# Kernel tuning notes

Hardware: AMD Instinct MI355X
Metric: run time of the kernel (lower is better)

Reference implementation:

```python
import jax, jax.numpy as jnp
import numpy as np

B, C, CI, H, W = 4, 64, 32, 96, 96  # batch, in_channels, inter_channels, spatial
EPS = 1e-5


def conv1x1(x, w, b):
    # x: [B,Cin,H,W], w: [Cout,Cin], b: [Cout]
    return jnp.einsum('bchw,oc->bohw', x, w) + b[None, :, None, None]


def maxpool2(x):
    b, c, h, w = x.shape
    return x.reshape(b, c, h // 2, 2, w // 2, 2).max(axis=(3, 5))


def setup_inputs() -> dict:
    key = jax.random.key(0)
    ks = jax.random.split(key, 12)
    s = 0.05  # keep unscaled attention logits in a sane range
    return {
        'x': jax.random.normal(ks[0], (B, C, H, W), jnp.float32),
        'feature': jax.random.normal(ks[1], (B, CI, H, W), jnp.float32),
        'g_w': jax.random.normal(ks[2], (C, C), jnp.float32) * s,
        'g_b': jax.random.normal(ks[3], (C,), jnp.float32) * s,
        'theta_w': jax.random.normal(ks[4], (C, C), jnp.float32) * s,
        'theta_b': jax.random.normal(ks[5], (C,), jnp.float32) * s,
        'phi_w': jax.random.normal(ks[6], (C, CI), jnp.float32) * s,
        'phi_b': jax.random.normal(ks[7], (C,), jnp.float32) * s,
        'W_w': jax.random.normal(ks[8], (CI, C), jnp.float32) * s,
        'W_b': jax.random.normal(ks[9], (CI,), jnp.float32) * s,
        'bn_gamma': jax.random.normal(ks[10], (CI,), jnp.float32) * s + 1.0,
        'bn_beta': jax.random.normal(ks[11], (CI,), jnp.float32) * s,
    }


def reference(x, feature, g_w, g_b, theta_w, theta_b, phi_w, phi_b, W_w, W_b, bn_gamma, bn_beta):
    b = x.shape[0]
    # g branch: conv1x1 then 2x2 maxpool -> [B, M, C]
    g_x = maxpool2(conv1x1(x, g_w, g_b)).reshape(b, C, -1).transpose(0, 2, 1)
    # theta: conv1x1 -> [B, N, C]
    theta_x = conv1x1(x, theta_w, theta_b).reshape(b, C, -1).transpose(0, 2, 1)
    # phi on `feature` (inter_channels -> in_channels) then maxpool -> [B, C, M]
    phi_f = maxpool2(conv1x1(feature, phi_w, phi_b)).reshape(b, C, -1)
    # unscaled attention: [B, N, M]
    f = jnp.einsum('bnc,bcm->bnm', theta_x, phi_f)
    f_div_C = jax.nn.softmax(f, axis=-1)
    y = jnp.einsum('bnm,bmc->bnc', f_div_C, g_x)  # [B, N, C]
    y = y.transpose(0, 2, 1).reshape(x.shape)
    z = y + x
    # W: conv1x1 (C -> CI) + BatchNorm2d (training mode, batch stats)
    z = conv1x1(z, W_w, W_b)
    mean = z.mean(axis=(0, 2, 3), keepdims=True)
    var = z.var(axis=(0, 2, 3), keepdims=True)
    z = (z - mean) * jax.lax.rsqrt(var + EPS)
    z = z * bn_gamma[None, :, None, None] + bn_beta[None, :, None, None]
    return z
```

## Files before the change

### kernel.cpp

```cpp
#include <hip/hip_runtime.h>
#include <hip/hip_bf16.h>

typedef __attribute__((ext_vector_type(8))) short short8;
typedef __attribute__((ext_vector_type(4))) float f32x4;
typedef __attribute__((ext_vector_type(4))) _Float16 half4;

#define NB 4
#define NN 9216
#define NM 2304

__device__ inline unsigned pk2(float a, float b) {
  __hip_bfloat16 ha = __float2bfloat16(a), hb = __float2bfloat16(b);
  return (unsigned)*(unsigned short*)&ha | ((unsigned)*(unsigned short*)&hb << 16);
}
__device__ inline float ubf(unsigned u) {
  unsigned v = u << 16; return *(float*)&v;
}
__device__ inline short8 pack8(const float* v) {
  short8 s;
#pragma unroll
  for (int j = 0; j < 8; ++j) { __hip_bfloat16 h = __float2bfloat16(v[j]); s[j] = *(short*)&h; }
  return s;
}
__device__ inline short8 ldw8(const float* p) {
  float tmp[8];
  *(float4*)&tmp[0] = *(const float4*)p;
  *(float4*)&tmp[4] = *(const float4*)(p + 4);
  return pack8(tmp);
}

__global__ __launch_bounds__(256, 3) void conv_pool_k(
    const float* __restrict__ x, const float* __restrict__ feat,
    const float* __restrict__ tw, const float* __restrict__ tbi,
    const float* __restrict__ gw, const float* __restrict__ gbi,
    const float* __restrict__ pw, const float* __restrict__ pbi,
    __hip_bfloat16* __restrict__ Theta, _Float16* __restrict__ Gcm,
    __hip_bfloat16* __restrict__ PhiT, float* __restrict__ psum) {
  __shared__ float xs[64][68];
  __shared__ float fs[64][36];
  int t = threadIdx.x, wv = t >> 6, lane = t & 63, l15 = lane & 15, q = lane >> 4;
  int b = blockIdx.y, bx = blockIdx.x;
  if (bx == 0 && b == 0 && t < 64) psum[t] = 0.f;
  int jt = bx % 3, rp = bx / 3;
  int i0 = rp * 2, j0 = jt * 32;
  int ot = wv;

  {
#pragma unroll
    for (int p = 0; p < 4; ++p) {
      int idx = p * 256 + t;
      int c = idx >> 4, s = idx & 15;
      int row = s >> 3, cl = (s & 7) * 4;
      float4 v = *(const float4*)(x + ((size_t)b * 64 + c) * NN + (i0 + row) * 96 + j0 + cl);
      int nl = row * 32 + cl;
      xs[nl][c] = v.x; xs[nl + 1][c] = v.y; xs[nl + 2][c] = v.z; xs[nl + 3][c] = v.w;
    }
#pragma unroll
    for (int p = 0; p < 2; ++p) {
      int idx = p * 256 + t;
      int c = idx >> 4, s = idx & 15;
      int row = s >> 3, cl = (s & 7) * 4;
      float4 v = *(const float4*)(feat + ((size_t)b * 32 + c) * NN + (i0 + row) * 96 + j0 + cl);
      int nl = row * 32 + cl;
      fs[nl][c] = v.x; fs[nl + 1][c] = v.y; fs[nl + 2][c] = v.z; fs[nl + 3][c] = v.w;
    }
  }

  short8 wt[2], wg[2], wp1;
#pragma unroll
  for (int kf = 0; kf < 2; ++kf) {
    wt[kf] = ldw8(tw + (size_t)(ot * 16 + l15) * 64 + kf * 32 + q * 8);
    wg[kf] = ldw8(gw + (size_t)(ot * 16 + l15) * 64 + kf * 32 + q * 8);
  }
  wp1 = ldw8(pw + (size_t)(ot * 16 + l15) * 32 + q * 8);

  __syncthreads();

  short8 bxf[4][2], bff[4];
  {
    float tmp[8];
#pragma unroll
    for (int tl = 0; tl < 4; ++tl) {
#pragma unroll
      for (int kf = 0; kf < 2; ++kf) {
        *(float4*)&tmp[0] = *(float4*)&xs[tl * 16 + l15][kf * 32 + q * 8];
        *(float4*)&tmp[4] = *(float4*)&xs[tl * 16 + l15][kf * 32 + q * 8 + 4];
        bxf[tl][kf] = pack8(tmp);
      }
      *(float4*)&tmp[0] = *(float4*)&fs[tl * 16 + l15][q * 8];
      *(float4*)&tmp[4] = *(float4*)&fs[tl * 16 + l15][q * 8 + 4];
      bff[tl] = pack8(tmp);
    }
  }

#pragma unroll
  for (int tl = 0; tl < 4; ++tl) {
    f32x4 d;
#pragma unroll
    for (int r = 0; r < 4; ++r) d[r] = tbi[ot * 16 + q * 4 + r];
    d = __builtin_amdgcn_mfma_f32_16x16x32_bf16(wt[0], bxf[tl][0], d, 0, 0, 0);
    d = __builtin_amdgcn_mfma_f32_16x16x32_bf16(wt[1], bxf[tl][1], d, 0, 0, 0);
    int n = (i0 + (tl >> 1)) * 96 + j0 + (tl & 1) * 16 + l15;
    size_t base = ((size_t)b * NN + n) * 64 + ot * 16 + q * 4;
    *(unsigned*)(Theta + base) = pk2(d[0], d[1]);
    *(unsigned*)(Theta + base + 2) = pk2(d[2], d[3]);
  }

  int mrow = rp * 48 + jt * 16;
  bool em = (l15 & 1) == 0;
#pragma unroll
  for (int ch = 0; ch < 2; ++ch) {
    f32x4 d0, d1;
#pragma unroll
    for (int r = 0; r < 4; ++r) { float bb = gbi[ot * 16 + q * 4 + r]; d0[r] = bb; d1[r] = bb; }
    d0 = __builtin_amdgcn_mfma_f32_16x16x32_bf16(wg[0], bxf[ch][0], d0, 0, 0, 0);
    d0 = __builtin_amdgcn_mfma_f32_16x16x32_bf16(wg[1], bxf[ch][1], d0, 0, 0, 0);
    d1 = __builtin_amdgcn_mfma_f32_16x16x32_bf16(wg[0], bxf[ch + 2][0], d1, 0, 0, 0);
    d1 = __builtin_amdgcn_mfma_f32_16x16x32_bf16(wg[1], bxf[ch + 2][1], d1, 0, 0, 0);
    float h[4];
#pragma unroll
    for (int r = 0; r < 4; ++r) {
      float v = fmaxf(d0[r], d1[r]);
      h[r] = fmaxf(v, __shfl_xor(v, 1));
    }
    if (em) {
      int m = mrow + ch * 8 + (l15 >> 1);
#pragma unroll
      for (int r = 0; r < 4; ++r)
        Gcm[((size_t)b * 64 + ot * 16 + q * 4 + r) * NM + m] = (_Float16)h[r];
    }
  }
#pragma unroll
  for (int ch = 0; ch < 2; ++ch) {
    f32x4 d0, d1;
#pragma unroll
    for (int r = 0; r < 4; ++r) { float bb = pbi[ot * 16 + q * 4 + r]; d0[r] = bb; d1[r] = bb; }
    d0 = __builtin_amdgcn_mfma_f32_16x16x32_bf16(wp1, bff[ch], d0, 0, 0, 0);
    d1 = __builtin_amdgcn_mfma_f32_16x16x32_bf16(wp1, bff[ch + 2], d1, 0, 0, 0);
    float h[4];
#pragma unroll
    for (int r = 0; r < 4; ++r) {
      float v = fmaxf(d0[r], d1[r]);
      h[r] = fmaxf(v, __shfl_xor(v, 1));
    }
    if (em) {
      int m = mrow + ch * 8 + (l15 >> 1);
      size_t base = ((size_t)b * NM + m) * 64 + ot * 16 + q * 4;
      *(unsigned*)(PhiT + base) = pk2(h[0], h[1]);
      *(unsigned*)(PhiT + base + 2) = pk2(h[2], h[3]);
    }
  }
}

__global__ __launch_bounds__(256, 3) void attn_k(
    const __hip_bfloat16* __restrict__ Theta, const __hip_bfloat16* __restrict__ PhiT,
    const _Float16* __restrict__ Gcm, const float* __restrict__ x,
    const float* __restrict__ Ww, const float* __restrict__ Wb,
    float* __restrict__ z2, float* __restrict__ psum) {
  __shared__ union {
    struct { __hip_bfloat16 phis[64][72]; _Float16 gs[64][72]; } st;
    struct { __hip_bfloat16 zpart[4][64][68]; __hip_bfloat16 zacc[64][72]; } ep;
  } u;
  __shared__ float rs[4][64];

  int t = threadIdx.x, wv = t >> 6, lane = t & 63;
  int l15 = lane & 15, q = lane >> 4;
  int b = blockIdx.y;
  int n0 = blockIdx.x * 64;

  short8 tb[4][2];
#pragma unroll
  for (int nt = 0; nt < 4; ++nt)
#pragma unroll
    for (int kf = 0; kf < 2; ++kf)
      tb[nt][kf] = *(const short8*)(Theta + ((size_t)b * NN + n0 + nt * 16 + l15) * 64 + kf * 32 + q * 8);

  f32x4 acc[4][4];
#pragma unroll
  for (int nt = 0; nt < 4; ++nt)
#pragma unroll
    for (int ct = 0; ct < 4; ++ct) acc[nt][ct] = (f32x4){0.f, 0.f, 0.f, 0.f};
  float rsum[4] = {0.f, 0.f, 0.f, 0.f};

  const __hip_bfloat16* phibase = PhiT + (size_t)b * NM * 64;
  const _Float16* gbase = Gcm + (size_t)b * 64 * NM;

  for (int ck = 0; ck < NM / 64; ++ck) {
    int m0 = ck * 64;
    __syncthreads();
#pragma unroll
    for (int p = 0; p < 2; ++p) {
      int idx = p * 256 + t, r = idx >> 3, seg = idx & 7;
      *(uint4*)&u.st.phis[r][seg * 8] = *(const uint4*)(phibase + (size_t)(m0 + r) * 64 + seg * 8);
    }
#pragma unroll
    for (int p = 0; p < 2; ++p) {
      int idx = p * 256 + t, c = idx >> 3, seg = idx & 7;
      *(uint4*)&u.st.gs[c][seg * 8] = *(const uint4*)(gbase + (size_t)c * NM + m0 + seg * 8);
    }
    __syncthreads();

    short8 pha[2];
#pragma unroll
    for (int kf = 0; kf < 2; ++kf)
      pha[kf] = *(const short8*)&u.st.phis[wv * 16 + l15][kf * 32 + q * 8];
    half4 gv[4];
#pragma unroll
    for (int ct = 0; ct < 4; ++ct)
      gv[ct] = *(const half4*)&u.st.gs[ct * 16 + l15][wv * 16 + q * 4];

    half4 pa[4];
#pragma unroll
    for (int nt = 0; nt < 4; ++nt) {
      f32x4 s = (f32x4){0.f, 0.f, 0.f, 0.f};
      s = __builtin_amdgcn_mfma_f32_16x16x32_bf16(pha[0], tb[nt][0], s, 0, 0, 0);
      s = __builtin_amdgcn_mfma_f32_16x16x32_bf16(pha[1], tb[nt][1], s, 0, 0, 0);
      float e0 = __expf(s[0]), e1 = __expf(s[1]), e2 = __expf(s[2]), e3 = __expf(s[3]);
      rsum[nt] += (e0 + e1) + (e2 + e3);
      pa[nt] = (half4){(_Float16)e0, (_Float16)e1, (_Float16)e2, (_Float16)e3};
    }
#pragma unroll
    for (int nt = 0; nt < 4; ++nt)
#pragma unroll
      for (int ct = 0; ct < 4; ++ct)
        acc[nt][ct] = __builtin_amdgcn_mfma_f32_16x16x16f16(pa[nt], gv[ct], acc[nt][ct], 0, 0, 0);
  }

#pragma unroll
  for (int nt = 0; nt < 4; ++nt) {
    float v = rsum[nt];
    v += __shfl_xor(v, 16);
    v += __shfl_xor(v, 32);
    if (lane < 16) rs[wv][nt * 16 + lane] = v;
  }
  __syncthreads();

#pragma unroll
  for (int nt = 0; nt < 4; ++nt)
#pragma unroll
    for (int ct = 0; ct < 4; ++ct)
#pragma unroll
      for (int r = 0; r < 4; ++r)
        u.ep.zpart[wv][nt * 16 + q * 4 + r][ct * 16 + l15] = __float2bfloat16(acc[nt][ct][r]);
  __syncthreads();

  {
    int row = wv * 16 + l15;
    float tot = rs[0][row] + rs[1][row] + rs[2][row] + rs[3][row];
    float rinv = 1.0f / tot;
    float ys[16];
#pragma unroll
    for (int j4 = 0; j4 < 4; ++j4) {
      uint2 p0 = *(const uint2*)&u.ep.zpart[0][row][q * 16 + j4 * 4];
      ys[j4 * 4 + 0] = ubf(p0.x & 0xffffu); ys[j4 * 4 + 1] = ubf(p0.x >> 16);
      ys[j4 * 4 + 2] = ubf(p0.y & 0xffffu); ys[j4 * 4 + 3] = ubf(p0.y >> 16);
    }
#pragma unroll
    for (int wvv = 1; wvv < 4; ++wvv) {
#pragma unroll
      for (int j4 = 0; j4 < 4; ++j4) {
        uint2 p0 = *(const uint2*)&u.ep.zpart[wvv][row][q * 16 + j4 * 4];
        ys[j4 * 4 + 0] += ubf(p0.x & 0xffffu); ys[j4 * 4 + 1] += ubf(p0.x >> 16);
        ys[j4 * 4 + 2] += ubf(p0.y & 0xffffu); ys[j4 * 4 + 3] += ubf(p0.y >> 16);
      }
    }
    float z1[16];
#pragma unroll
    for (int i = 0; i < 16; ++i)
      z1[i] = ys[i] * rinv + x[((size_t)b * 64 + q * 16 + i) * NN + n0 + row];
#pragma unroll
    for (int i2 = 0; i2 < 8; ++i2)
      *(unsigned*)&u.ep.zacc[row][q * 16 + 2 * i2] = pk2(z1[2 * i2], z1[2 * i2 + 1]);
  }
  __syncthreads();

  int nw = n0 + wv * 16;
  short8 wbf[2][2];
#pragma unroll
  for (int ot = 0; ot < 2; ++ot)
#pragma unroll
    for (int kf = 0; kf < 2; ++kf)
      wbf[ot][kf] = ldw8(Ww + (size_t)(ot * 16 + l15) * 64 + kf * 32 + q * 8);
  short8 za0 = *(const short8*)&u.ep.zacc[wv * 16 + l15][q * 8];
  short8 za1 = *(const short8*)&u.ep.zacc[wv * 16 + l15][32 + q * 8];

  f32x4 dd[2];
#pragma unroll
  for (int ot = 0; ot < 2; ++ot) {
    float bias = Wb[ot * 16 + l15];
    f32x4 d = (f32x4){bias, bias, bias, bias};
    d = __builtin_amdgcn_mfma_f32_16x16x32_bf16(za0, wbf[ot][0], d, 0, 0, 0);
    d = __builtin_amdgcn_mfma_f32_16x16x32_bf16(za1, wbf[ot][1], d, 0, 0, 0);
#pragma unroll
    for (int r = 0; r < 4; ++r)
      z2[((size_t)b * NN + nw + q * 4 + r) * 32 + ot * 16 + l15] = d[r];
    dd[ot] = d;
  }

  __syncthreads();
#pragma unroll
  for (int ot = 0; ot < 2; ++ot) {
    float ps = (dd[ot][0] + dd[ot][1]) + (dd[ot][2] + dd[ot][3]);
    float ps2 = dd[ot][0] * dd[ot][0] + dd[ot][1] * dd[ot][1] +
                dd[ot][2] * dd[ot][2] + dd[ot][3] * dd[ot][3];
    ps += __shfl_xor(ps, 16);  ps += __shfl_xor(ps, 32);
    ps2 += __shfl_xor(ps2, 16); ps2 += __shfl_xor(ps2, 32);
    if (lane < 16) {
      rs[wv][ot * 16 + lane] = ps;
      rs[wv][32 + ot * 16 + lane] = ps2;
    }
  }
  __syncthreads();
  if (t < 64) {
    float tot = rs[0][t] + rs[1][t] + rs[2][t] + rs[3][t];
    atomicAdd(&psum[t], tot);
  }
}

__global__ __launch_bounds__(256) void bn_apply(
    const float* __restrict__ z2, const float* __restrict__ psum,
    const float* __restrict__ gamma, const float* __restrict__ beta,
    float* __restrict__ out) {
  __shared__ float ssl[64];
  __shared__ float zt[32][65];
  int t = threadIdx.x, b = blockIdx.y, n0 = blockIdx.x * 64;
  if (t < 32) {
    const float inv = 1.0f / (float)(NB * NN);
    float mean = psum[t] * inv;
    float var = psum[32 + t] * inv - mean * mean;
    float sc = gamma[t] * rsqrtf(var + 1e-5f);
    ssl[t] = sc;
    ssl[32 + t] = beta[t] - mean * sc;
  }
#pragma unroll
  for (int it = 0; it < 2; ++it) {
    int idx = it * 256 + t, r = idx >> 3, seg = idx & 7;
    float4 vv = *(const float4*)(z2 + ((size_t)b * NN + n0 + r) * 32 + seg * 4);
    zt[seg * 4 + 0][r] = vv.x; zt[seg * 4 + 1][r] = vv.y;
    zt[seg * 4 + 2][r] = vv.z; zt[seg * 4 + 3][r] = vv.w;
  }
  __syncthreads();
  int o = t >> 3, nseg = t & 7;
  float sc = ssl[o], sh = ssl[32 + o];
  float4 a, c;
  a.x = zt[o][nseg * 8 + 0] * sc + sh; a.y = zt[o][nseg * 8 + 1] * sc + sh;
  a.z = zt[o][nseg * 8 + 2] * sc + sh; a.w = zt[o][nseg * 8 + 3] * sc + sh;
  c.x = zt[o][nseg * 8 + 4] * sc + sh; c.y = zt[o][nseg * 8 + 5] * sc + sh;
  c.z = zt[o][nseg * 8 + 6] * sc + sh; c.w = zt[o][nseg * 8 + 7] * sc + sh;
  float* po = out + ((size_t)b * 32 + o) * NN + n0 + nseg * 8;
  *(float4*)po = a;
  *(float4*)(po + 4) = c;
}

extern "C" void kernel_launch(void* const* d_in, const int* in_sizes, int n_in,
                              void* d_out, int out_size, void* d_ws, size_t ws_size,
                              hipStream_t stream) {
  const float* x       = (const float*)d_in[0];
  const float* feature = (const float*)d_in[1];
  const float* g_w     = (const float*)d_in[2];
  const float* g_b     = (const float*)d_in[3];
  const float* theta_w = (const float*)d_in[4];
  const float* theta_b = (const float*)d_in[5];
  const float* phi_w   = (const float*)d_in[6];
  const float* phi_b   = (const float*)d_in[7];
  const float* W_w     = (const float*)d_in[8];
  const float* W_b     = (const float*)d_in[9];
  const float* bn_g    = (const float*)d_in[10];
  const float* bn_b    = (const float*)d_in[11];

  char* ws = (char*)d_ws;
  __hip_bfloat16* Theta = (__hip_bfloat16*)(ws);
  _Float16*       Gcm   = (_Float16*)(ws + 4718592);
  __hip_bfloat16* PhiT  = (__hip_bfloat16*)(ws + 5898240);
  float*          z2    = (float*)(ws + 7077888);
  float*          psum  = (float*)(ws + 11796480);

  conv_pool_k<<<dim3(144, NB), dim3(256), 0, stream>>>(
      x, feature, theta_w, theta_b, g_w, g_b, phi_w, phi_b, Theta, Gcm, PhiT, psum);
  attn_k<<<dim3(144, NB), dim3(256), 0, stream>>>(
      Theta, PhiT, Gcm, x, W_w, W_b, z2, psum);
  bn_apply<<<dim3(144, NB), dim3(256), 0, stream>>>(
      z2, psum, bn_g, bn_b, (float*)d_out);
}
```

Before: 148.8 us.

## Fuse three kernels into one persistent kernel with software grid barriers

```diff
diff --git a/kernel.cpp b/kernel.cpp
--- a/kernel.cpp
+++ b/kernel.cpp
@@ -8,6 +8,7 @@
 #define NB 4
 #define NN 9216
 #define NM 2304
+#define NBLK (144 * NB)
 
 __device__ inline unsigned pk2(float a, float b) {
   __hip_bfloat16 ha = __float2bfloat16(a), hb = __float2bfloat16(b);
@@ -29,23 +30,46 @@
   return pack8(tmp);
 }
 
-__global__ __launch_bounds__(256, 3) void conv_pool_k(
+__device__ inline void gridbar(unsigned* c, unsigned target) {
+  __syncthreads();
+  __threadfence();
+  if (threadIdx.x == 0) {
+    atomicAdd(c, 1u);
+    while (atomicAdd(c, 0u) < target) __builtin_amdgcn_s_sleep(8);
+  }
+  __syncthreads();
+  __threadfence();
+}
+
+__global__ __launch_bounds__(256, 3) void mega_k(
     const float* __restrict__ x, const float* __restrict__ feat,
     const float* __restrict__ tw, const float* __restrict__ tbi,
     const float* __restrict__ gw, const float* __restrict__ gbi,
     const float* __restrict__ pw, const float* __restrict__ pbi,
+    const float* __restrict__ Ww, const float* __restrict__ Wb,
+    const float* __restrict__ gamma, const float* __restrict__ beta,
     __hip_bfloat16* __restrict__ Theta, _Float16* __restrict__ Gcm,
-    __hip_bfloat16* __restrict__ PhiT, float* __restrict__ psum) {
-  __shared__ float xs[64][68];
-  __shared__ float fs[64][36];
-  int t = threadIdx.x, wv = t >> 6, lane = t & 63, l15 = lane & 15, q = lane >> 4;
+    __hip_bfloat16* __restrict__ PhiT,
+    unsigned* __restrict__ ctr, float* __restrict__ psum,
+    float* __restrict__ out) {
+  __shared__ union {
+    struct { float xs[64][68]; float fs[64][36]; } cv;
+    struct { __hip_bfloat16 phis[64][72]; _Float16 gs[64][72]; } st;
+    struct { __hip_bfloat16 zpart[4][64][68]; __hip_bfloat16 zacc[64][72]; } ep;
+    float zt[32][68];
+  } u;
+  __shared__ float rs[4][64];
+  __shared__ float ssl[64];
+
+  int t = threadIdx.x, wv = t >> 6, lane = t & 63;
+  int l15 = lane & 15, q = lane >> 4;
   int b = blockIdx.y, bx = blockIdx.x;
-  if (bx == 0 && b == 0 && t < 64) psum[t] = 0.f;
-  int jt = bx % 3, rp = bx / 3;
-  int i0 = rp * 2, j0 = jt * 32;
-  int ot = wv;
 
   {
+    int jt = bx % 3, rp = bx / 3;
+    int i0 = rp * 2, j0 = jt * 32;
+    int ot = wv;
+
 #pragma unroll
     for (int p = 0; p < 4; ++p) {
       int idx = p * 256 + t;
@@ -53,7 +77,8 @@
       int row = s >> 3, cl = (s & 7) * 4;
       float4 v = *(const float4*)(x + ((size_t)b * 64 + c) * NN + (i0 + row) * 96 + j0 + cl);
       int nl = row * 32 + cl;
-      xs[nl][c] = v.x; xs[nl + 1][c] = v.y; xs[nl + 2][c] = v.z; xs[nl + 3][c] = v.w;
+      u.cv.xs[nl][c] = v.x; u.cv.xs[nl + 1][c] = v.y;
+      u.cv.xs[nl + 2][c] = v.z; u.cv.xs[nl + 3][c] = v.w;
     }
 #pragma unroll
     for (int p = 0; p < 2; ++p) {
@@ -62,294 +87,276 @@
       int row = s >> 3, cl = (s & 7) * 4;
       float4 v = *(const float4*)(feat + ((size_t)b * 32 + c) * NN + (i0 + row) * 96 + j0 + cl);
       int nl = row * 32 + cl;
-      fs[nl][c] = v.x; fs[nl + 1][c] = v.y; fs[nl + 2][c] = v.z; fs[nl + 3][c] = v.w;
+      u.cv.fs[nl][c] = v.x; u.cv.fs[nl + 1][c] = v.y;
+      u.cv.fs[nl + 2][c] = v.z; u.cv.fs[nl + 3][c] = v.w;
+    }
+
+    short8 wt[2], wg[2], wp1;
+#pragma unroll
+    for (int kf = 0; kf < 2; ++kf) {
+      wt[kf] = ldw8(tw + (size_t)(ot * 16 + l15) * 64 + kf * 32 + q * 8);
+      wg[kf] = ldw8(gw + (size_t)(ot * 16 + l15) * 64 + kf * 32 + q * 8);
+    }
+    wp1 = ldw8(pw + (size_t)(ot * 16 + l15) * 32 + q * 8);
+
+    __syncthreads();
+
+    short8 bxf[4][2], bff[4];
+    {
+      float tmp[8];
+#pragma unroll
+      for (int tl = 0; tl < 4; ++tl) {
+#pragma unroll
+        for (int kf = 0; kf < 2; ++kf) {
+          *(float4*)&tmp[0] = *(float4*)&u.cv.xs[tl * 16 + l15][kf * 32 + q * 8];
+          *(float4*)&tmp[4] = *(float4*)&u.cv.xs[tl * 16 + l15][kf * 32 + q * 8 + 4];
+          bxf[tl][kf] = pack8(tmp);
+        }
+        *(float4*)&tmp[0] = *(float4*)&u.cv.fs[tl * 16 + l15][q * 8];
+        *(float4*)&tmp[4] = *(float4*)&u.cv.fs[tl * 16 + l15][q * 8 + 4];
+        bff[tl] = pack8(tmp);
+      }
+    }
+
+#pragma unroll
+    for (int tl = 0; tl < 4; ++tl) {
+      f32x4 d;
+#pragma unroll
+      for (int r = 0; r < 4; ++r) d[r] = tbi[ot * 16 + q * 4 + r];
+      d = __builtin_amdgcn_mfma_f32_16x16x32_bf16(wt[0], bxf[tl][0], d, 0, 0, 0);
+      d = __builtin_amdgcn_mfma_f32_16x16x32_bf16(wt[1], bxf[tl][1], d, 0, 0, 0);
+      int n = (i0 + (tl >> 1)) * 96 + j0 + (tl & 1) * 16 + l15;
+      size_t base = ((size_t)b * NN + n) * 64 + ot * 16 + q * 4;
+      *(unsigned*)(Theta + base) = pk2(d[0], d[1]);
+      *(unsigned*)(Theta + base + 2) = pk2(d[2], d[3]);
+    }
+
+    int mrow = rp * 48 + jt * 16;
+    bool em = (l15 & 1) == 0;
+#pragma unroll
+    for (int ch = 0; ch < 2; ++ch) {
+      f32x4 d0, d1;
+#pragma unroll
+      for (int r = 0; r < 4; ++r) { float bb = gbi[ot * 16 + q * 4 + r]; d0[r] = bb; d1[r] = bb; }
+      d0 = __builtin_amdgcn_mfma_f32_16x16x32_bf16(wg[0], bxf[ch][0], d0, 0, 0, 0);
+      d0 = __builtin_amdgcn_mfma_f32_16x16x32_bf16(wg[1], bxf[ch][1], d0, 0, 0, 0);
+      d1 = __builtin_amdgcn_mfma_f32_16x16x32_bf16(wg[0], bxf[ch + 2][0], d1, 0, 0, 0);
+      d1 = __builtin_amdgcn_mfma_f32_16x16x32_bf16(wg[1], bxf[ch + 2][1], d1, 0, 0, 0);
+      float h[4];
+#pragma unroll
+      for (int r = 0; r < 4; ++r) {
+        float v = fmaxf(d0[r], d1[r]);
+        h[r] = fmaxf(v, __shfl_xor(v, 1));
+      }
+      if (em) {
+        int m = mrow + ch * 8 + (l15 >> 1);
+#pragma unroll
+        for (int r = 0; r < 4; ++r)
+          Gcm[((size_t)b * 64 + ot * 16 + q * 4 + r) * NM + m] = (_Float16)h[r];
+      }
+    }
+#pragma unroll
+    for (int ch = 0; ch < 2; ++ch) {
+      f32x4 d0, d1;
+#pragma unroll
+      for (int r = 0; r < 4; ++r) { float bb = pbi[ot * 16 + q * 4 + r]; d0[r] = bb; d1[r] = bb; }
+      d0 = __builtin_amdgcn_mfma_f32_16x16x32_bf16(wp1, bff[ch], d0, 0, 0, 0);
+      d1 = __builtin_amdgcn_mfma_f32_16x16x32_bf16(wp1, bff[ch + 2], d1, 0, 0, 0);
+      float h[4];
+#pragma unroll
+      for (int r = 0; r < 4; ++r) {
+        float v = fmaxf(d0[r], d1[r]);
+        h[r] = fmaxf(v, __shfl_xor(v, 1));
+      }
+      if (em) {
+        int m = mrow + ch * 8 + (l15 >> 1);
+        size_t base = ((size_t)b * NM + m) * 64 + ot * 16 + q * 4;
+        *(unsigned*)(PhiT + base) = pk2(h[0], h[1]);
+        *(unsigned*)(PhiT + base + 2) = pk2(h[2], h[3]);
+      }
     }
   }
 
-  short8 wt[2], wg[2], wp1;
-#pragma unroll
-  for (int kf = 0; kf < 2; ++kf) {
-    wt[kf] = ldw8(tw + (size_t)(ot * 16 + l15) * 64 + kf * 32 + q * 8);
-    wg[kf] = ldw8(gw + (size_t)(ot * 16 + l15) * 64 + kf * 32 + q * 8);
+  gridbar(ctr, NBLK);
+
+  f32x4 dd[2];
+  {
+    int n0 = bx * 64;
+
+    short8 tb[4][2];
+#pragma unroll
+    for (int nt = 0; nt < 4; ++nt)
+#pragma unroll
+      for (int kf = 0; kf < 2; ++kf)
+        tb[nt][kf] = *(const short8*)(Theta + ((size_t)b * NN + n0 + nt * 16 + l15) * 64 + kf * 32 + q * 8);
+
+    f32x4 acc[4][4];
+#pragma unroll
+    for (int nt = 0; nt < 4; ++nt)
+#pragma unroll
+      for (int ct = 0; ct < 4; ++ct) acc[nt][ct] = (f32x4){0.f, 0.f, 0.f, 0.f};
+    float rsum[4] = {0.f, 0.f, 0.f, 0.f};
+
+    const __hip_bfloat16* phibase = PhiT + (size_t)b * NM * 64;
+    const _Float16* gbase = Gcm + (size_t)b * 64 * NM;
+
+    for (int ck = 0; ck < NM / 64; ++ck) {
+      int m0 = ck * 64;
+      __syncthreads();
+#pragma unroll
+      for (int p = 0; p < 2; ++p) {
+        int idx = p * 256 + t, r = idx >> 3, seg = idx & 7;
+        *(uint4*)&u.st.phis[r][seg * 8] = *(const uint4*)(phibase + (size_t)(m0 + r) * 64 + seg * 8);
+      }
+#pragma unroll
+      for (int p = 0; p < 2; ++p) {
+        int idx = p * 256 + t, c = idx >> 3, seg = idx & 7;
+        *(uint4*)&u.st.gs[c][seg * 8] = *(const uint4*)(gbase + (size_t)c * NM + m0 + seg * 8);
+      }
+      __syncthreads();
+
+      short8 pha[2];
+#pragma unroll
+      for (int kf = 0; kf < 2; ++kf)
+        pha[kf] = *(const short8*)&u.st.phis[wv * 16 + l15][kf * 32 + q * 8];
+      half4 gv[4];
+#pragma unroll
+      for (int ct = 0; ct < 4; ++ct)
+        gv[ct] = *(const half4*)&u.st.gs[ct * 16 + l15][wv * 16 + q * 4];
+
+      half4 pa[4];
+#pragma unroll
+      for (int nt = 0; nt < 4; ++nt) {
+        f32x4 s = (f32x4){0.f, 0.f, 0.f, 0.f};
+        s = __builtin_amdgcn_mfma_f32_16x16x32_bf16(pha[0], tb[nt][0], s, 0, 0, 0);
+        s = __builtin_amdgcn_mfma_f32_16x16x32_bf16(pha[1], tb[nt][1], s, 0, 0, 0);
+        float e0 = __expf(s[0]), e1 = __expf(s[1]), e2 = __expf(s[2]), e3 = __expf(s[3]);
+        rsum[nt] += (e0 + e1) + (e2 + e3);
+        pa[nt] = (half4){(_Float16)e0, (_Float16)e1, (_Float16)e2, (_Float16)e3};
+      }
+#pragma unroll
+      for (int nt = 0; nt < 4; ++nt)
+#pragma unroll
+        for (int ct = 0; ct < 4; ++ct)
+          acc[nt][ct] = __builtin_amdgcn_mfma_f32_16x16x16f16(pa[nt], gv[ct], acc[nt][ct], 0, 0, 0);
+    }
+
+#pragma unroll
+    for (int nt = 0; nt < 4; ++nt) {
+      float v = rsum[nt];
+      v += __shfl_xor(v, 16);
+      v += __shfl_xor(v, 32);
+      if (lane < 16) rs[wv][nt * 16 + lane] = v;
+    }
+    __syncthreads();
+
+#pragma unroll
+    for (int nt = 0; nt < 4; ++nt)
+#pragma unroll
+      for (int ct = 0; ct < 4; ++ct)
+#pragma unroll
+        for (int r = 0; r < 4; ++r)
+          u.ep.zpart[wv][nt * 16 + q * 4 + r][ct * 16 + l15] = __float2bfloat16(acc[nt][ct][r]);
+    __syncthreads();
+
+    {
+      int row = wv * 16 + l15;
+      float tot = rs[0][row] + rs[1][row] + rs[2][row] + rs[3][row];
+      float rinv = 1.0f / tot;
+      float ys[16];
+#pragma unroll
+      for (int j4 = 0; j4 < 4; ++j4) {
+        uint2 p0 = *(const uint2*)&u.ep.zpart[0][row][q * 16 + j4 * 4];
+        ys[j4 * 4 + 0] = ubf(p0.x & 0xffffu); ys[j4 * 4 + 1] = ubf(p0.x >> 16);
+        ys[j4 * 4 + 2] = ubf(p0.y & 0xffffu); ys[j4 * 4 + 3] = ubf(p0.y >> 16);
+      }
+#pragma unroll
+      for (int wvv = 1; wvv < 4; ++wvv) {
+#pragma unroll
+        for (int j4 = 0; j4 < 4; ++j4) {
+          uint2 p0 = *(const uint2*)&u.ep.zpart[wvv][row][q * 16 + j4 * 4];
+          ys[j4 * 4 + 0] += ubf(p0.x & 0xffffu); ys[j4 * 4 + 1] += ubf(p0.x >> 16);
+          ys[j4 * 4 + 2] += ubf(p0.y & 0xffffu); ys[j4 * 4 + 3] += ubf(p0.y >> 16);
+        }
+      }
+      float z1[16];
+#pragma unroll
+      for (int i = 0; i < 16; ++i)
+        z1[i] = ys[i] * rinv + x[((size_t)b * 64 + q * 16 + i) * NN + n0 + row];
+#pragma unroll
+      for (int i2 = 0; i2 < 8; ++i2)
+        *(unsigned*)&u.ep.zacc[row][q * 16 + 2 * i2] = pk2(z1[2 * i2], z1[2 * i2 + 1]);
+    }
+    __syncthreads();
+
+    short8 wbf[2][2];
+#pragma unroll
+    for (int ot = 0; ot < 2; ++ot)
+#pragma unroll
+      for (int kf = 0; kf < 2; ++kf)
+        wbf[ot][kf] = ldw8(Ww + (size_t)(ot * 16 + l15) * 64 + kf * 32 + q * 8);
+    short8 za0 = *(const short8*)&u.ep.zacc[wv * 16 + l15][q * 8];
+    short8 za1 = *(const short8*)&u.ep.zacc[wv * 16 + l15][32 + q * 8];
+
+#pragma unroll
+    for (int ot = 0; ot < 2; ++ot) {
+      float bias = Wb[ot * 16 + l15];
+      f32x4 d = (f32x4){bias, bias, bias, bias};
+      d = __builtin_amdgcn_mfma_f32_16x16x32_bf16(za0, wbf[ot][0], d, 0, 0, 0);
+      d = __builtin_amdgcn_mfma_f32_16x16x32_bf16(za1, wbf[ot][1], d, 0, 0, 0);
+      dd[ot] = d;
+    }
+
+    __syncthreads();
+#pragma unroll
+    for (int ot = 0; ot < 2; ++ot) {
+      float ps = (dd[ot][0] + dd[ot][1]) + (dd[ot][2] + dd[ot][3]);
+      float ps2 = dd[ot][0] * dd[ot][0] + dd[ot][1] * dd[ot][1] +
+                  dd[ot][2] * dd[ot][2] + dd[ot][3] * dd[ot][3];
+      ps += __shfl_xor(ps, 16);  ps += __shfl_xor(ps, 32);
+      ps2 += __shfl_xor(ps2, 16); ps2 += __shfl_xor(ps2, 32);
+      if (lane < 16) {
+        rs[wv][ot * 16 + lane] = ps;
+        rs[wv][32 + ot * 16 + lane] = ps2;
+      }
+    }
+    __syncthreads();
+    if (t < 64) {
+      float tot = rs[0][t] + rs[1][t] + rs[2][t] + rs[3][t];
+      atomicAdd(&psum[t], tot);
+    }
   }
-  wp1 = ldw8(pw + (size_t)(ot * 16 + l15) * 32 + q * 8);
-
-  __syncthreads();
-
-  short8 bxf[4][2], bff[4];
+
+  gridbar(ctr + 1, NBLK);
+
   {
-    float tmp[8];
-#pragma unroll
-    for (int tl = 0; tl < 4; ++tl) {
-#pragma unroll
-      for (int kf = 0; kf < 2; ++kf) {
-        *(float4*)&tmp[0] = *(float4*)&xs[tl * 16 + l15][kf * 32 + q * 8];
-        *(float4*)&tmp[4] = *(float4*)&xs[tl * 16 + l15][kf * 32 + q * 8 + 4];
-        bxf[tl][kf] = pack8(tmp);
-      }
-      *(float4*)&tmp[0] = *(float4*)&fs[tl * 16 + l15][q * 8];
-      *(float4*)&tmp[4] = *(float4*)&fs[tl * 16 + l15][q * 8 + 4];
-      bff[tl] = pack8(tmp);
-    }
+    int n0 = bx * 64;
+    if (t < 32) {
+      const float inv = 1.0f / (float)(NB * NN);
+      float mean = psum[t] * inv;
+      float var = psum[32 + t] * inv - mean * mean;
+      float sc = gamma[t] * rsqrtf(var + 1e-5f);
+      ssl[t] = sc;
+      ssl[32 + t] = beta[t] - mean * sc;
+    }
+#pragma unroll
+    for (int ot = 0; ot < 2; ++ot)
+#pragma unroll
+      for (int r = 0; r < 4; ++r)
+        u.zt[ot * 16 + l15][wv * 16 + q * 4 + r] = dd[ot][r];
+    __syncthreads();
+
+    int o = t >> 3, nseg = t & 7;
+    float sc = ssl[o], sh = ssl[32 + o];
+    float4 a, c;
+    a.x = u.zt[o][nseg * 8 + 0] * sc + sh; a.y = u.zt[o][nseg * 8 + 1] * sc + sh;
+    a.z = u.zt[o][nseg * 8 + 2] * sc + sh; a.w = u.zt[o][nseg * 8 + 3] * sc + sh;
+    c.x = u.zt[o][nseg * 8 + 4] * sc + sh; c.y = u.zt[o][nseg * 8 + 5] * sc + sh;
+    c.z = u.zt[o][nseg * 8 + 6] * sc + sh; c.w = u.zt[o][nseg * 8 + 7] * sc + sh;
+    float* po = out + ((size_t)b * 32 + o) * NN + n0 + nseg * 8;
+    *(float4*)po = a;
+    *(float4*)(po + 4) = c;
   }
-
-#pragma unroll
-  for (int tl = 0; tl < 4; ++tl) {
-    f32x4 d;
-#pragma unroll
-    for (int r = 0; r < 4; ++r) d[r] = tbi[ot * 16 + q * 4 + r];
-    d = __builtin_amdgcn_mfma_f32_16x16x32_bf16(wt[0], bxf[tl][0], d, 0, 0, 0);
-    d = __builtin_amdgcn_mfma_f32_16x16x32_bf16(wt[1], bxf[tl][1], d, 0, 0, 0);
-    int n = (i0 + (tl >> 1)) * 96 + j0 + (tl & 1) * 16 + l15;
-    size_t base = ((size_t)b * NN + n) * 64 + ot * 16 + q * 4;
-    *(unsigned*)(Theta + base) = pk2(d[0], d[1]);
-    *(unsigned*)(Theta + base + 2) = pk2(d[2], d[3]);
-  }
-
-  int mrow = rp * 48 + jt * 16;
-  bool em = (l15 & 1) == 0;
-#pragma unroll
-  for (int ch = 0; ch < 2; ++ch) {
-    f32x4 d0, d1;
-#pragma unroll
-    for (int r = 0; r < 4; ++r) { float bb = gbi[ot * 16 + q * 4 + r]; d0[r] = bb; d1[r] = bb; }
-    d0 = __builtin_amdgcn_mfma_f32_16x16x32_bf16(wg[0], bxf[ch][0], d0, 0, 0, 0);
-    d0 = __builtin_amdgcn_mfma_f32_16x16x32_bf16(wg[1], bxf[ch][1], d0, 0, 0, 0);
-    d1 = __builtin_amdgcn_mfma_f32_16x16x32_bf16(wg[0], bxf[ch + 2][0], d1, 0, 0, 0);
-    d1 = __builtin_amdgcn_mfma_f32_16x16x32_bf16(wg[1], bxf[ch + 2][1], d1, 0, 0, 0);
-    float h[4];
-#pragma unroll
-    for (int r = 0; r < 4; ++r) {
-      float v = fmaxf(d0[r], d1[r]);
-      h[r] = fmaxf(v, __shfl_xor(v, 1));
-    }
-    if (em) {
-      int m = mrow + ch * 8 + (l15 >> 1);
-#pragma unroll
-      for (int r = 0; r < 4; ++r)
-        Gcm[((size_t)b * 64 + ot * 16 + q * 4 + r) * NM + m] = (_Float16)h[r];
-    }
-  }
-#pragma unroll
-  for (int ch = 0; ch < 2; ++ch) {
-    f32x4 d0, d1;
-#pragma unroll
-    for (int r = 0; r < 4; ++r) { float bb = pbi[ot * 16 + q * 4 + r]; d0[r] = bb; d1[r] = bb; }
-    d0 = __builtin_amdgcn_mfma_f32_16x16x32_bf16(wp1, bff[ch], d0, 0, 0, 0);
-    d1 = __builtin_amdgcn_mfma_f32_16x16x32_bf16(wp1, bff[ch + 2], d1, 0, 0, 0);
-    float h[4];
-#pragma unroll
-    for (int r = 0; r < 4; ++r) {
-      float v = fmaxf(d0[r], d1[r]);
-      h[r] = fmaxf(v, __shfl_xor(v, 1));
-    }
-    if (em) {
-      int m = mrow + ch * 8 + (l15 >> 1);
-      size_t base = ((size_t)b * NM + m) * 64 + ot * 16 + q * 4;
-      *(unsigned*)(PhiT + base) = pk2(h[0], h[1]);
-      *(unsigned*)(PhiT + base + 2) = pk2(h[2], h[3]);
-    }
-  }
-}
-
-__global__ __launch_bounds__(256, 3) void attn_k(
-    const __hip_bfloat16* __restrict__ Theta, const __hip_bfloat16* __restrict__ PhiT,
-    const _Float16* __restrict__ Gcm, const float* __restrict__ x,
-    const float* __restrict__ Ww, const float* __restrict__ Wb,
-    float* __restrict__ z2, float* __restrict__ psum) {
-  __shared__ union {
-    struct { __hip_bfloat16 phis[64][72]; _Float16 gs[64][72]; } st;
-    struct { __hip_bfloat16 zpart[4][64][68]; __hip_bfloat16 zacc[64][72]; } ep;
-  } u;
-  __shared__ float rs[4][64];
-
-  int t = threadIdx.x, wv = t >> 6, lane = t & 63;
-  int l15 = lane & 15, q = lane >> 4;
-  int b = blockIdx.y;
-  int n0 = blockIdx.x * 64;
-
-  short8 tb[4][2];
-#pragma unroll
-  for (int nt = 0; nt < 4; ++nt)
-#pragma unroll
-    for (int kf = 0; kf < 2; ++kf)
-      tb[nt][kf] = *(const short8*)(Theta + ((size_t)b * NN + n0 + nt * 16 + l15) * 64 + kf * 32 + q * 8);
-
-  f32x4 acc[4][4];
-#pragma unroll
-  for (int nt = 0; nt < 4; ++nt)
-#pragma unroll
-    for (int ct = 0; ct < 4; ++ct) acc[nt][ct] = (f32x4){0.f, 0.f, 0.f, 0.f};
-  float rsum[4] = {0.f, 0.f, 0.f, 0.f};
-
-  const __hip_bfloat16* phibase = PhiT + (size_t)b * NM * 64;
-  const _Float16* gbase = Gcm + (size_t)b * 64 * NM;
-
-  for (int ck = 0; ck < NM / 64; ++ck) {
-    int m0 = ck * 64;
-    __syncthreads();
-#pragma unroll
-    for (int p = 0; p < 2; ++p) {
-      int idx = p * 256 + t, r = idx >> 3, seg = idx & 7;
-      *(uint4*)&u.st.phis[r][seg * 8] = *(const uint4*)(phibase + (size_t)(m0 + r) * 64 + seg * 8);
-    }
-#pragma unroll
-    for (int p = 0; p < 2; ++p) {
-      int idx = p * 256 + t, c = idx >> 3, seg = idx & 7;
-      *(uint4*)&u.st.gs[c][seg * 8] = *(const uint4*)(gbase + (size_t)c * NM + m0 + seg * 8);
-    }
-    __syncthreads();
-
-    short8 pha[2];
-#pragma unroll
-    for (int kf = 0; kf < 2; ++kf)
-      pha[kf] = *(const short8*)&u.st.phis[wv * 16 + l15][kf * 32 + q * 8];
-    half4 gv[4];
-#pragma unroll
-    for (int ct = 0; ct < 4; ++ct)
-      gv[ct] = *(const half4*)&u.st.gs[ct * 16 + l15][wv * 16 + q * 4];
-
-    half4 pa[4];
-#pragma unroll
-    for (int nt = 0; nt < 4; ++nt) {
-      f32x4 s = (f32x4){0.f, 0.f, 0.f, 0.f};
-      s = __builtin_amdgcn_mfma_f32_16x16x32_bf16(pha[0], tb[nt][0], s, 0, 0, 0);
-      s = __builtin_amdgcn_mfma_f32_16x16x32_bf16(pha[1], tb[nt][1], s, 0, 0, 0);
-      float e0 = __expf(s[0]), e1 = __expf(s[1]), e2 = __expf(s[2]), e3 = __expf(s[3]);
-      rsum[nt] += (e0 + e1) + (e2 + e3);
-      pa[nt] = (half4){(_Float16)e0, (_Float16)e1, (_Float16)e2, (_Float16)e3};
-    }
-#pragma unroll
-    for (int nt = 0; nt < 4; ++nt)
-#pragma unroll
-      for (int ct = 0; ct < 4; ++ct)
-        acc[nt][ct] = __builtin_amdgcn_mfma_f32_16x16x16f16(pa[nt], gv[ct], acc[nt][ct], 0, 0, 0);
-  }
-
-#pragma unroll
-  for (int nt = 0; nt < 4; ++nt) {
-    float v = rsum[nt];
-    v += __shfl_xor(v, 16);
-    v += __shfl_xor(v, 32);
-    if (lane < 16) rs[wv][nt * 16 + lane] = v;
-  }
-  __syncthreads();
-
-#pragma unroll
-  for (int nt = 0; nt < 4; ++nt)
-#pragma unroll
-    for (int ct = 0; ct < 4; ++ct)
-#pragma unroll
-      for (int r = 0; r < 4; ++r)
-        u.ep.zpart[wv][nt * 16 + q * 4 + r][ct * 16 + l15] = __float2bfloat16(acc[nt][ct][r]);
-  __syncthreads();
-
-  {
-    int row = wv * 16 + l15;
-    float tot = rs[0][row] + rs[1][row] + rs[2][row] + rs[3][row];
-    float rinv = 1.0f / tot;
-    float ys[16];
-#pragma unroll
-    for (int j4 = 0; j4 < 4; ++j4) {
-      uint2 p0 = *(const uint2*)&u.ep.zpart[0][row][q * 16 + j4 * 4];
-      ys[j4 * 4 + 0] = ubf(p0.x & 0xffffu); ys[j4 * 4 + 1] = ubf(p0.x >> 16);
-      ys[j4 * 4 + 2] = ubf(p0.y & 0xffffu); ys[j4 * 4 + 3] = ubf(p0.y >> 16);
-    }
-#pragma unroll
-    for (int wvv = 1; wvv < 4; ++wvv) {
-#pragma unroll
-      for (int j4 = 0; j4 < 4; ++j4) {
-        uint2 p0 = *(const uint2*)&u.ep.zpart[wvv][row][q * 16 + j4 * 4];
-        ys[j4 * 4 + 0] += ubf(p0.x & 0xffffu); ys[j4 * 4 + 1] += ubf(p0.x >> 16);
-        ys[j4 * 4 + 2] += ubf(p0.y & 0xffffu); ys[j4 * 4 + 3] += ubf(p0.y >> 16);
-      }
-    }
-    float z1[16];
-#pragma unroll
-    for (int i = 0; i < 16; ++i)
-      z1[i] = ys[i] * rinv + x[((size_t)b * 64 + q * 16 + i) * NN + n0 + row];
-#pragma unroll
-    for (int i2 = 0; i2 < 8; ++i2)
-      *(unsigned*)&u.ep.zacc[row][q * 16 + 2 * i2] = pk2(z1[2 * i2], z1[2 * i2 + 1]);
-  }
-  __syncthreads();
-
-  int nw = n0 + wv * 16;
-  short8 wbf[2][2];
-#pragma unroll
-  for (int ot = 0; ot < 2; ++ot)
-#pragma unroll
-    for (int kf = 0; kf < 2; ++kf)
-      wbf[ot][kf] = ldw8(Ww + (size_t)(ot * 16 + l15) * 64 + kf * 32 + q * 8);
-  short8 za0 = *(const short8*)&u.ep.zacc[wv * 16 + l15][q * 8];
-  short8 za1 = *(const short8*)&u.ep.zacc[wv * 16 + l15][32 + q * 8];
-
-  f32x4 dd[2];
-#pragma unroll
-  for (int ot = 0; ot < 2; ++ot) {
-    float bias = Wb[ot * 16 + l15];
-    f32x4 d = (f32x4){bias, bias, bias, bias};
-    d = __builtin_amdgcn_mfma_f32_16x16x32_bf16(za0, wbf[ot][0], d, 0, 0, 0);
-    d = __builtin_amdgcn_mfma_f32_16x16x32_bf16(za1, wbf[ot][1], d, 0, 0, 0);
-#pragma unroll
-    for (int r = 0; r < 4; ++r)
-      z2[((size_t)b * NN + nw + q * 4 + r) * 32 + ot * 16 + l15] = d[r];
-    dd[ot] = d;
-  }
-
-  __syncthreads();
-#pragma unroll
-  for (int ot = 0; ot < 2; ++ot) {
-    float ps = (dd[ot][0] + dd[ot][1]) + (dd[ot][2] + dd[ot][3]);
-    float ps2 = dd[ot][0] * dd[ot][0] + dd[ot][1] * dd[ot][1] +
-                dd[ot][2] * dd[ot][2] + dd[ot][3] * dd[ot][3];
-    ps += __shfl_xor(ps, 16);  ps += __shfl_xor(ps, 32);
-    ps2 += __shfl_xor(ps2, 16); ps2 += __shfl_xor(ps2, 32);
-    if (lane < 16) {
-      rs[wv][ot * 16 + lane] = ps;
-      rs[wv][32 + ot * 16 + lane] = ps2;
-    }
-  }
-  __syncthreads();
-  if (t < 64) {
-    float tot = rs[0][t] + rs[1][t] + rs[2][t] + rs[3][t];
-    atomicAdd(&psum[t], tot);
-  }
-}
-
-__global__ __launch_bounds__(256) void bn_apply(
-    const float* __restrict__ z2, const float* __restrict__ psum,
-    const float* __restrict__ gamma, const float* __restrict__ beta,
-    float* __restrict__ out) {
-  __shared__ float ssl[64];
-  __shared__ float zt[32][65];
-  int t = threadIdx.x, b = blockIdx.y, n0 = blockIdx.x * 64;
-  if (t < 32) {
-    const float inv = 1.0f / (float)(NB * NN);
-    float mean = psum[t] * inv;
-    float var = psum[32 + t] * inv - mean * mean;
-    float sc = gamma[t] * rsqrtf(var + 1e-5f);
-    ssl[t] = sc;
-    ssl[32 + t] = beta[t] - mean * sc;
-  }
-#pragma unroll
-  for (int it = 0; it < 2; ++it) {
-    int idx = it * 256 + t, r = idx >> 3, seg = idx & 7;
-    float4 vv = *(const float4*)(z2 + ((size_t)b * NN + n0 + r) * 32 + seg * 4);
-    zt[seg * 4 + 0][r] = vv.x; zt[seg * 4 + 1][r] = vv.y;
-    zt[seg * 4 + 2][r] = vv.z; zt[seg * 4 + 3][r] = vv.w;
-  }
-  __syncthreads();
-  int o = t >> 3, nseg = t & 7;
-  float sc = ssl[o], sh = ssl[32 + o];
-  float4 a, c;
-  a.x = zt[o][nseg * 8 + 0] * sc + sh; a.y = zt[o][nseg * 8 + 1] * sc + sh;
-  a.z = zt[o][nseg * 8 + 2] * sc + sh; a.w = zt[o][nseg * 8 + 3] * sc + sh;
-  c.x = zt[o][nseg * 8 + 4] * sc + sh; c.y = zt[o][nseg * 8 + 5] * sc + sh;
-  c.z = zt[o][nseg * 8 + 6] * sc + sh; c.w = zt[o][nseg * 8 + 7] * sc + sh;
-  float* po = out + ((size_t)b * 32 + o) * NN + n0 + nseg * 8;
-  *(float4*)po = a;
-  *(float4*)(po + 4) = c;
 }
 
 extern "C" void kernel_launch(void* const* d_in, const int* in_sizes, int n_in,
@@ -372,13 +379,11 @@
   __hip_bfloat16* Theta = (__hip_bfloat16*)(ws);
   _Float16*       Gcm   = (_Float16*)(ws + 4718592);
   __hip_bfloat16* PhiT  = (__hip_bfloat16*)(ws + 5898240);
-  float*          z2    = (float*)(ws + 7077888);
-  float*          psum  = (float*)(ws + 11796480);
-
-  conv_pool_k<<<dim3(144, NB), dim3(256), 0, stream>>>(
-      x, feature, theta_w, theta_b, g_w, g_b, phi_w, phi_b, Theta, Gcm, PhiT, psum);
-  attn_k<<<dim3(144, NB), dim3(256), 0, stream>>>(
-      Theta, PhiT, Gcm, x, W_w, W_b, z2, psum);
-  bn_apply<<<dim3(144, NB), dim3(256), 0, stream>>>(
-      z2, psum, bn_g, bn_b, (float*)d_out);
-}
+  unsigned*       ctr   = (unsigned*)(ws + 7077888);
+  float*          psum  = (float*)(ws + 7078144);
+
+  hipMemsetAsync(ws + 7077888, 0, 512, stream);
+  mega_k<<<dim3(144, NB), dim3(256), 0, stream>>>(
+      x, feature, theta_w, theta_b, g_w, g_b, phi_w, phi_b, W_w, W_b,
+      bn_g, bn_b, Theta, Gcm, PhiT, ctr, psum, (float*)d_out);
+}
```

After: 379.7 us. +155.2%, slower.

## Double-buffer attention K/V tiles and drop LDS staging in conv kernel

Applied to the files above, without the earlier changes.

```diff
diff --git a/kernel.cpp b/kernel.cpp
--- a/kernel.cpp
+++ b/kernel.cpp
@@ -29,42 +29,20 @@
   return pack8(tmp);
 }
 
-__global__ __launch_bounds__(256, 3) void conv_pool_k(
+__global__ __launch_bounds__(256) void conv_pool_k(
     const float* __restrict__ x, const float* __restrict__ feat,
     const float* __restrict__ tw, const float* __restrict__ tbi,
     const float* __restrict__ gw, const float* __restrict__ gbi,
     const float* __restrict__ pw, const float* __restrict__ pbi,
     __hip_bfloat16* __restrict__ Theta, _Float16* __restrict__ Gcm,
     __hip_bfloat16* __restrict__ PhiT, float* __restrict__ psum) {
-  __shared__ float xs[64][68];
-  __shared__ float fs[64][36];
   int t = threadIdx.x, wv = t >> 6, lane = t & 63, l15 = lane & 15, q = lane >> 4;
   int b = blockIdx.y, bx = blockIdx.x;
   if (bx == 0 && b == 0 && t < 64) psum[t] = 0.f;
-  int jt = bx % 3, rp = bx / 3;
-  int i0 = rp * 2, j0 = jt * 32;
+  int jt = bx % 6, rp = bx / 6;
+  int i0 = rp * 2, j0 = jt * 16;
+  int ntop = i0 * 96 + j0;
   int ot = wv;
-
-  {
-#pragma unroll
-    for (int p = 0; p < 4; ++p) {
-      int idx = p * 256 + t;
-      int c = idx >> 4, s = idx & 15;
-      int row = s >> 3, cl = (s & 7) * 4;
-      float4 v = *(const float4*)(x + ((size_t)b * 64 + c) * NN + (i0 + row) * 96 + j0 + cl);
-      int nl = row * 32 + cl;
-      xs[nl][c] = v.x; xs[nl + 1][c] = v.y; xs[nl + 2][c] = v.z; xs[nl + 3][c] = v.w;
-    }
-#pragma unroll
-    for (int p = 0; p < 2; ++p) {
-      int idx = p * 256 + t;
-      int c = idx >> 4, s = idx & 15;
-      int row = s >> 3, cl = (s & 7) * 4;
-      float4 v = *(const float4*)(feat + ((size_t)b * 32 + c) * NN + (i0 + row) * 96 + j0 + cl);
-      int nl = row * 32 + cl;
-      fs[nl][c] = v.x; fs[nl + 1][c] = v.y; fs[nl + 2][c] = v.z; fs[nl + 3][c] = v.w;
-    }
-  }
 
   short8 wt[2], wg[2], wp1;
 #pragma unroll
@@ -74,49 +52,47 @@
   }
   wp1 = ldw8(pw + (size_t)(ot * 16 + l15) * 32 + q * 8);
 
-  __syncthreads();
-
-  short8 bxf[4][2], bff[4];
+  short8 bxf[2][2], bff[2];
   {
     float tmp[8];
 #pragma unroll
-    for (int tl = 0; tl < 4; ++tl) {
+    for (int row = 0; row < 2; ++row) {
 #pragma unroll
       for (int kf = 0; kf < 2; ++kf) {
-        *(float4*)&tmp[0] = *(float4*)&xs[tl * 16 + l15][kf * 32 + q * 8];
-        *(float4*)&tmp[4] = *(float4*)&xs[tl * 16 + l15][kf * 32 + q * 8 + 4];
-        bxf[tl][kf] = pack8(tmp);
+#pragma unroll
+        for (int j = 0; j < 8; ++j)
+          tmp[j] = x[((size_t)b * 64 + kf * 32 + q * 8 + j) * NN + ntop + row * 96 + l15];
+        bxf[row][kf] = pack8(tmp);
       }
-      *(float4*)&tmp[0] = *(float4*)&fs[tl * 16 + l15][q * 8];
-      *(float4*)&tmp[4] = *(float4*)&fs[tl * 16 + l15][q * 8 + 4];
-      bff[tl] = pack8(tmp);
-    }
-  }
-
-#pragma unroll
-  for (int tl = 0; tl < 4; ++tl) {
+#pragma unroll
+      for (int j = 0; j < 8; ++j)
+        tmp[j] = feat[((size_t)b * 32 + q * 8 + j) * NN + ntop + row * 96 + l15];
+      bff[row] = pack8(tmp);
+    }
+  }
+
+  int m = rp * 48 + ((j0 + l15) >> 1);
+  bool em = (l15 & 1) == 0;
+
+#pragma unroll
+  for (int row = 0; row < 2; ++row) {
     f32x4 d;
 #pragma unroll
     for (int r = 0; r < 4; ++r) d[r] = tbi[ot * 16 + q * 4 + r];
-    d = __builtin_amdgcn_mfma_f32_16x16x32_bf16(wt[0], bxf[tl][0], d, 0, 0, 0);
-    d = __builtin_amdgcn_mfma_f32_16x16x32_bf16(wt[1], bxf[tl][1], d, 0, 0, 0);
-    int n = (i0 + (tl >> 1)) * 96 + j0 + (tl & 1) * 16 + l15;
-    size_t base = ((size_t)b * NN + n) * 64 + ot * 16 + q * 4;
+    d = __builtin_amdgcn_mfma_f32_16x16x32_bf16(wt[0], bxf[row][0], d, 0, 0, 0);
+    d = __builtin_amdgcn_mfma_f32_16x16x32_bf16(wt[1], bxf[row][1], d, 0, 0, 0);
+    size_t base = ((size_t)b * NN + ntop + row * 96 + l15) * 64 + ot * 16 + q * 4;
     *(unsigned*)(Theta + base) = pk2(d[0], d[1]);
     *(unsigned*)(Theta + base + 2) = pk2(d[2], d[3]);
   }
-
-  int mrow = rp * 48 + jt * 16;
-  bool em = (l15 & 1) == 0;
-#pragma unroll
-  for (int ch = 0; ch < 2; ++ch) {
+  {
     f32x4 d0, d1;
 #pragma unroll
     for (int r = 0; r < 4; ++r) { float bb = gbi[ot * 16 + q * 4 + r]; d0[r] = bb; d1[r] = bb; }
-    d0 = __builtin_amdgcn_mfma_f32_16x16x32_bf16(wg[0], bxf[ch][0], d0, 0, 0, 0);
-    d0 = __builtin_amdgcn_mfma_f32_16x16x32_bf16(wg[1], bxf[ch][1], d0, 0, 0, 0);
-    d1 = __builtin_amdgcn_mfma_f32_16x16x32_bf16(wg[0], bxf[ch + 2][0], d1, 0, 0, 0);
-    d1 = __builtin_amdgcn_mfma_f32_16x16x32_bf16(wg[1], bxf[ch + 2][1], d1, 0, 0, 0);
+    d0 = __builtin_amdgcn_mfma_f32_16x16x32_bf16(wg[0], bxf[0][0], d0, 0, 0, 0);
+    d0 = __builtin_amdgcn_mfma_f32_16x16x32_bf16(wg[1], bxf[0][1], d0, 0, 0, 0);
+    d1 = __builtin_amdgcn_mfma_f32_16x16x32_bf16(wg[0], bxf[1][0], d1, 0, 0, 0);
+    d1 = __builtin_amdgcn_mfma_f32_16x16x32_bf16(wg[1], bxf[1][1], d1, 0, 0, 0);
     float h[4];
 #pragma unroll
     for (int r = 0; r < 4; ++r) {
@@ -124,19 +100,17 @@
       h[r] = fmaxf(v, __shfl_xor(v, 1));
     }
     if (em) {
-      int m = mrow + ch * 8 + (l15 >> 1);
 #pragma unroll
       for (int r = 0; r < 4; ++r)
         Gcm[((size_t)b * 64 + ot * 16 + q * 4 + r) * NM + m] = (_Float16)h[r];
     }
   }
-#pragma unroll
-  for (int ch = 0; ch < 2; ++ch) {
+  {
     f32x4 d0, d1;
 #pragma unroll
     for (int r = 0; r < 4; ++r) { float bb = pbi[ot * 16 + q * 4 + r]; d0[r] = bb; d1[r] = bb; }
-    d0 = __builtin_amdgcn_mfma_f32_16x16x32_bf16(wp1, bff[ch], d0, 0, 0, 0);
-    d1 = __builtin_amdgcn_mfma_f32_16x16x32_bf16(wp1, bff[ch + 2], d1, 0, 0, 0);
+    d0 = __builtin_amdgcn_mfma_f32_16x16x32_bf16(wp1, bff[0], d0, 0, 0, 0);
+    d1 = __builtin_amdgcn_mfma_f32_16x16x32_bf16(wp1, bff[1], d1, 0, 0, 0);
     float h[4];
 #pragma unroll
     for (int r = 0; r < 4; ++r) {
@@ -144,7 +118,6 @@
       h[r] = fmaxf(v, __shfl_xor(v, 1));
     }
     if (em) {
-      int m = mrow + ch * 8 + (l15 >> 1);
       size_t base = ((size_t)b * NM + m) * 64 + ot * 16 + q * 4;
       *(unsigned*)(PhiT + base) = pk2(h[0], h[1]);
       *(unsigned*)(PhiT + base + 2) = pk2(h[2], h[3]);
@@ -158,7 +131,7 @@
     const float* __restrict__ Ww, const float* __restrict__ Wb,
     float* __restrict__ z2, float* __restrict__ psum) {
   __shared__ union {
-    struct { __hip_bfloat16 phis[64][72]; _Float16 gs[64][72]; } st;
+    struct { __hip_bfloat16 phis[2][64][72]; _Float16 gs[2][64][72]; } st;
     struct { __hip_bfloat16 zpart[4][64][68]; __hip_bfloat16 zacc[64][72]; } ep;
   } u;
   __shared__ float rs[4][64];
@@ -185,29 +158,44 @@
   const __hip_bfloat16* phibase = PhiT + (size_t)b * NM * 64;
   const _Float16* gbase = Gcm + (size_t)b * 64 * NM;
 
+  int pr = t >> 3, pseg = t & 7;
+  uint4 rphi[2], rg[2];
+
+#pragma unroll
+  for (int p = 0; p < 2; ++p)
+    rphi[p] = *(const uint4*)(phibase + (size_t)(p * 32 + pr) * 64 + pseg * 8);
+#pragma unroll
+  for (int p = 0; p < 2; ++p)
+    rg[p] = *(const uint4*)(gbase + (size_t)(p * 32 + pr) * NM + pseg * 8);
+#pragma unroll
+  for (int p = 0; p < 2; ++p)
+    *(uint4*)&u.st.phis[0][p * 32 + pr][pseg * 8] = rphi[p];
+#pragma unroll
+  for (int p = 0; p < 2; ++p)
+    *(uint4*)&u.st.gs[0][p * 32 + pr][pseg * 8] = rg[p];
+
   for (int ck = 0; ck < NM / 64; ++ck) {
-    int m0 = ck * 64;
+    int cur = ck & 1;
     __syncthreads();
-#pragma unroll
-    for (int p = 0; p < 2; ++p) {
-      int idx = p * 256 + t, r = idx >> 3, seg = idx & 7;
-      *(uint4*)&u.st.phis[r][seg * 8] = *(const uint4*)(phibase + (size_t)(m0 + r) * 64 + seg * 8);
-    }
-#pragma unroll
-    for (int p = 0; p < 2; ++p) {
-      int idx = p * 256 + t, c = idx >> 3, seg = idx & 7;
-      *(uint4*)&u.st.gs[c][seg * 8] = *(const uint4*)(gbase + (size_t)c * NM + m0 + seg * 8);
-    }
-    __syncthreads();
+
+    if (ck < 35) {
+      int m1 = (ck + 1) * 64;
+#pragma unroll
+      for (int p = 0; p < 2; ++p)
+        rphi[p] = *(const uint4*)(phibase + (size_t)(m1 + p * 32 + pr) * 64 + pseg * 8);
+#pragma unroll
+      for (int p = 0; p < 2; ++p)
+        rg[p] = *(const uint4*)(gbase + (size_t)(p * 32 + pr) * NM + m1 + pseg * 8);
+    }
 
     short8 pha[2];
 #pragma unroll
     for (int kf = 0; kf < 2; ++kf)
-      pha[kf] = *(const short8*)&u.st.phis[wv * 16 + l15][kf * 32 + q * 8];
+      pha[kf] = *(const short8*)&u.st.phis[cur][wv * 16 + l15][kf * 32 + q * 8];
     half4 gv[4];
 #pragma unroll
     for (int ct = 0; ct < 4; ++ct)
-      gv[ct] = *(const half4*)&u.st.gs[ct * 16 + l15][wv * 16 + q * 4];
+      gv[ct] = *(const half4*)&u.st.gs[cur][ct * 16 + l15][wv * 16 + q * 4];
 
     half4 pa[4];
 #pragma unroll
@@ -224,6 +212,15 @@
 #pragma unroll
       for (int ct = 0; ct < 4; ++ct)
         acc[nt][ct] = __builtin_amdgcn_mfma_f32_16x16x16f16(pa[nt], gv[ct], acc[nt][ct], 0, 0, 0);
+
+    if (ck < 35) {
+#pragma unroll
+      for (int p = 0; p < 2; ++p)
+        *(uint4*)&u.st.phis[cur ^ 1][p * 32 + pr][pseg * 8] = rphi[p];
+#pragma unroll
+      for (int p = 0; p < 2; ++p)
+        *(uint4*)&u.st.gs[cur ^ 1][p * 32 + pr][pseg * 8] = rg[p];
+    }
   }
 
 #pragma unroll
@@ -375,7 +372,7 @@
   float*          z2    = (float*)(ws + 7077888);
   float*          psum  = (float*)(ws + 11796480);
 
-  conv_pool_k<<<dim3(144, NB), dim3(256), 0, stream>>>(
+  conv_pool_k<<<dim3(288, NB), dim3(256), 0, stream>>>(
       x, feature, theta_w, theta_b, g_w, g_b, phi_w, phi_b, Theta, Gcm, PhiT, psum);
   attn_k<<<dim3(144, NB), dim3(256), 0, stream>>>(
       Theta, PhiT, Gcm, x, W_w, W_b, z2, psum);
```

Measured after the change: 142.7 us. 1.04x faster.
